# Kernel optimization log

Measured on AMD Instinct MI355X. Metric: run time of the kernel, lower is better.

The kernel has to match this reference:

```python
import jax
import jax.numpy as jnp
import numpy as np
from jax import lax

B, T, D = 32, 256, 512   # batch, seq len, controller_dim (== memory_dim)
S = 2048                 # memory_slots
EPS_LN = 1e-5            # nn.LayerNorm default eps
EPS_NRM = 1e-12          # F.normalize default eps


def setup_inputs() -> dict:
    key = jax.random.key(0)
    ks = jax.random.split(key, 12)
    sc = 1.0 / np.sqrt(D)  # roughly torch Linear init scale
    return {
        "controller_seq": jax.random.normal(ks[0], (B, T, D), dtype=jnp.float32),
        "memory": jax.random.normal(ks[1], (S, D), dtype=jnp.float32),
        "Wk": jax.random.normal(ks[2], (D, D), dtype=jnp.float32) * sc,
        "bk": jax.random.normal(ks[3], (D,), dtype=jnp.float32) * sc,
        "We": jax.random.normal(ks[4], (D, D), dtype=jnp.float32) * sc,
        "be": jax.random.normal(ks[5], (D,), dtype=jnp.float32) * sc,
        "Ww": jax.random.normal(ks[6], (D, D), dtype=jnp.float32) * sc,
        "bw": jax.random.normal(ks[7], (D,), dtype=jnp.float32) * sc,
        "Wg": jax.random.normal(ks[8], (D, D), dtype=jnp.float32) * sc,
        "bg": jax.random.normal(ks[9], (D,), dtype=jnp.float32) * sc,
        "gamma": jnp.ones((D,), dtype=jnp.float32),
        "beta": jnp.zeros((D,), dtype=jnp.float32),
    }


def _l2norm(x, axis=-1):
    # matches F.normalize: x / max(||x||, eps)
    n = jnp.sqrt(jnp.sum(x * x, axis=axis, keepdims=True))
    return x / jnp.maximum(n, EPS_NRM)


def _layernorm(x, gamma, beta):
    mu = jnp.mean(x, axis=-1, keepdims=True)
    var = jnp.mean((x - mu) ** 2, axis=-1, keepdims=True)
    return (x - mu) * lax.rsqrt(var + EPS_LN) * gamma + beta


def reference(controller_seq, memory, Wk, bk, We, be, Ww, bw, Wg, bg, gamma, beta):
    batch = controller_seq.shape[0]

    def step(mem, c):  # mem: [S, Dm], c: [B, Dc]
        # --- read (addressing by cosine similarity) ---
        k = c @ Wk.T + bk                       # [B, Dm]
        sim = _l2norm(k) @ _l2norm(mem).T       # [B, S]
        w = jax.nn.softmax(sim, axis=-1)        # [B, S]
        read_val = w @ mem                      # [B, Dm]
        # --- write (erase / add, averaged over batch) ---
        erase = jax.nn.sigmoid(c @ We.T + be)   # [B, Dm]
        add = c @ Ww.T + bw                     # [B, Dm]
        # mean_b (1 - w_bs * e_bd) = 1 - (w^T e)/B ; avoids [B,S,Dm] intermediate
        erase_m = 1.0 - jnp.einsum("bs,bd->sd", w, erase) / batch
        add_m = jnp.einsum("bs,bd->sd", w, add) / batch
        new_mem = _layernorm(mem * erase_m + add_m, gamma, beta)  # dropout in eval mode
        # --- gated output ---
        g = jax.nn.sigmoid(c @ Wg.T + bg)       # [B, Dm]
        out_t = g * c + (1.0 - g) * read_val
        return new_mem, out_t

    _, outs = lax.scan(step, memory, jnp.swapaxes(controller_seq, 0, 1))  # outs: [T, B, D]
    return jnp.swapaxes(outs, 0, 1)  # [B, T, D]
```

## Files before the change

kernel.cpp:

```cpp
#include <hip/hip_runtime.h>

#define DEV __device__ __forceinline__

namespace {
constexpr int Bc = 32;
constexpr int Tc = 256;
constexpr int Dc = 512;
constexpr int NBLK = 256;
constexpr int NW   = 128;
constexpr int ROWS = 16;

constexpr size_t OFF_KN   = 0;
constexpr size_t OFF_E    = OFF_KN + (size_t)Tc * Bc * Dc;
constexpr size_t OFF_A    = OFF_E  + (size_t)Tc * Bc * Dc;
constexpr size_t OFF_RP   = OFF_A  + (size_t)Tc * Bc * Dc;
constexpr size_t OFF_DENP = OFF_RP + (size_t)2 * NW * Bc * Dc;
constexpr size_t OFF_FLAGS= OFF_DENP + (size_t)2 * NW * Bc;
}

DEV float sigm(float x) { return 1.0f / (1.0f + __expf(-x)); }

DEV float ld1cg(const float* p) {
  unsigned u = __hip_atomic_load((const unsigned*)p, __ATOMIC_RELAXED,
                                 __HIP_MEMORY_SCOPE_AGENT);
  return __uint_as_float(u);
}
DEV void st1cg(float* p, float v) {
  __hip_atomic_store((unsigned*)p, __float_as_uint(v), __ATOMIC_RELAXED,
                     __HIP_MEMORY_SCOPE_AGENT);
}
DEV unsigned long long ld8cg(const unsigned long long* p) {
  return __hip_atomic_load(p, __ATOMIC_RELAXED, __HIP_MEMORY_SCOPE_AGENT);
}
DEV void st8cg(unsigned long long* p, unsigned long long v) {
  __hip_atomic_store(p, v, __ATOMIC_RELAXED, __HIP_MEMORY_SCOPE_AGENT);
}

DEV unsigned pack_bf2(float x, float y) {
  unsigned ux = __float_as_uint(x), uy = __float_as_uint(y);
  unsigned rx = (ux + 0x7FFFu + ((ux >> 16) & 1u)) >> 16;
  unsigned ry = (uy + 0x7FFFu + ((uy >> 16) & 1u)) >> 16;
  return rx | (ry << 16);
}
DEV float lo16f(unsigned u) { return __uint_as_float(u << 16); }
DEV float hi16f(unsigned u) { return __uint_as_float(u & 0xFFFF0000u); }

__global__ __launch_bounds__(256) void k_gemm(
    const float* __restrict__ A,
    const float* __restrict__ Wk, const float* __restrict__ bk,
    const float* __restrict__ We, const float* __restrict__ be,
    const float* __restrict__ Ww, const float* __restrict__ bw,
    const float* __restrict__ Wg, const float* __restrict__ bg,
    float* __restrict__ ws, float* __restrict__ gout)
{
  __shared__ float As[32][68];
  __shared__ float Bs[32][68];

  const int bid = blockIdx.x;
  const int mat = bid >> 10;
  const int rem = bid & 1023;
  const int rt = rem >> 3, jt = rem & 7;
  const int rbase = rt * 64, jbase = jt * 64;

  const float* Wm; const float* bm;
  if      (mat == 0) { Wm = Wk; bm = bk; }
  else if (mat == 1) { Wm = We; bm = be; }
  else if (mat == 2) { Wm = Ww; bm = bw; }
  else               { Wm = Wg; bm = bg; }

  const int tid = threadIdx.x;
  const int lr = tid >> 2;
  const int lk = (tid & 3) * 8;
  const int ty = tid >> 4, tx = tid & 15;

  float acc[4][4] = {};

  for (int k0 = 0; k0 < Dc; k0 += 32) {
    const float4 a0 = *(const float4*)&A [(size_t)(rbase + lr) * Dc + k0 + lk];
    const float4 a1 = *(const float4*)&A [(size_t)(rbase + lr) * Dc + k0 + lk + 4];
    const float4 b0 = *(const float4*)&Wm[(size_t)(jbase + lr) * Dc + k0 + lk];
    const float4 b1 = *(const float4*)&Wm[(size_t)(jbase + lr) * Dc + k0 + lk + 4];
    __syncthreads();
    As[lk + 0][lr] = a0.x; As[lk + 1][lr] = a0.y; As[lk + 2][lr] = a0.z; As[lk + 3][lr] = a0.w;
    As[lk + 4][lr] = a1.x; As[lk + 5][lr] = a1.y; As[lk + 6][lr] = a1.z; As[lk + 7][lr] = a1.w;
    Bs[lk + 0][lr] = b0.x; Bs[lk + 1][lr] = b0.y; Bs[lk + 2][lr] = b0.z; Bs[lk + 3][lr] = b0.w;
    Bs[lk + 4][lr] = b1.x; Bs[lk + 5][lr] = b1.y; Bs[lk + 6][lr] = b1.z; Bs[lk + 7][lr] = b1.w;
    __syncthreads();
    #pragma unroll
    for (int kk = 0; kk < 32; ++kk) {
      const float4 av = *(const float4*)&As[kk][ty * 4];
      const float4 bv = *(const float4*)&Bs[kk][tx * 4];
      const float ar[4] = {av.x, av.y, av.z, av.w};
      const float br[4] = {bv.x, bv.y, bv.z, bv.w};
      #pragma unroll
      for (int i = 0; i < 4; ++i)
        #pragma unroll
        for (int j = 0; j < 4; ++j)
          acc[i][j] = fmaf(ar[i], br[j], acc[i][j]);
    }
  }

  const float4 bias = *(const float4*)&bm[jbase + tx * 4];
  const float bi[4] = {bias.x, bias.y, bias.z, bias.w};
  #pragma unroll
  for (int i = 0; i < 4; ++i) {
    const int r = rbase + ty * 4 + i;
    float v[4];
    #pragma unroll
    for (int j = 0; j < 4; ++j) {
      v[j] = acc[i][j] + bi[j];
      if (mat & 1) v[j] = sigm(v[j]);
    }
    float4 o; o.x = v[0]; o.y = v[1]; o.z = v[2]; o.w = v[3];
    if (mat == 3) {
      *(float4*)&gout[(size_t)r * Dc + jbase + tx * 4] = o;
    } else {
      float* dst = ws + (mat == 0 ? OFF_KN : (mat == 1 ? OFF_E : OFF_A));
      const int t = r & 255, b = r >> 8;
      *(float4*)&dst[((size_t)t * Bc + b) * Dc + jbase + tx * 4] = o;
    }
  }
}

__global__ __launch_bounds__(256) void k_knorm(float* __restrict__ kn)
{
  const int row = blockIdx.x * 4 + (threadIdx.x >> 6);
  const int lane = threadIdx.x & 63;
  float* p = kn + (size_t)row * Dc;
  float4 v0 = *(const float4*)&p[lane * 4];
  float4 v1 = *(const float4*)&p[256 + lane * 4];
  float ss = v0.x*v0.x + v0.y*v0.y + v0.z*v0.z + v0.w*v0.w
           + v1.x*v1.x + v1.y*v1.y + v1.z*v1.z + v1.w*v1.w;
  #pragma unroll
  for (int off = 32; off >= 1; off >>= 1) ss += __shfl_xor(ss, off);
  const float inv = 1.0f / fmaxf(sqrtf(ss), 1e-12f);
  v0.x *= inv; v0.y *= inv; v0.z *= inv; v0.w *= inv;
  v1.x *= inv; v1.y *= inv; v1.z *= inv; v1.w *= inv;
  *(float4*)&p[lane * 4] = v0;
  *(float4*)&p[256 + lane * 4] = v1;
}

DEV void gbar(unsigned* flags, unsigned step, int bid, int tid)
{
  __syncthreads();
  if (tid == 0)
    __hip_atomic_store(&flags[bid * 16], step, __ATOMIC_RELAXED,
                       __HIP_MEMORY_SCOPE_AGENT);
  while (__hip_atomic_load(&flags[tid * 16], __ATOMIC_RELAXED,
                           __HIP_MEMORY_SCOPE_AGENT) < step)
    __builtin_amdgcn_s_sleep(1);
  __syncthreads();
}

DEV void sim_phase(const float* __restrict__ knp, float* __restrict__ denp_row,
                   const float (*y)[516], float* __restrict__ ew_own,
                   const float* invn_s, float* sred, int tid)
{
  const int r = tid >> 4, bp = tid & 15;
  const float* k0p = knp + (size_t)bp * Dc;
  const float* k1p = knp + (size_t)(bp + 16) * Dc;
  float acc0 = 0.f, acc1 = 0.f;
  #pragma unroll 4
  for (int dq = 0; dq < Dc / 4; ++dq) {
    const float4 y4 = *(const float4*)&y[r][dq * 4];
    const float4 ka = *(const float4*)&k0p[dq * 4];
    const float4 kb = *(const float4*)&k1p[dq * 4];
    acc0 = fmaf(y4.x, ka.x, acc0); acc0 = fmaf(y4.y, ka.y, acc0);
    acc0 = fmaf(y4.z, ka.z, acc0); acc0 = fmaf(y4.w, ka.w, acc0);
    acc1 = fmaf(y4.x, kb.x, acc1); acc1 = fmaf(y4.y, kb.y, acc1);
    acc1 = fmaf(y4.z, kb.z, acc1); acc1 = fmaf(y4.w, kb.w, acc1);
  }
  const float iv = invn_s[r];
  const float e0 = __expf(acc0 * iv);
  const float e1 = __expf(acc1 * iv);
  ew_own[r * 32 + bp]      = e0;
  ew_own[r * 32 + bp + 16] = e1;
  if (tid < 32) sred[tid] = 0.f;
  __syncthreads();
  atomicAdd(&sred[bp], e0);
  atomicAdd(&sred[bp + 16], e1);
  __syncthreads();
  if (tid < 32) st1cg(&denp_row[tid], sred[tid]);
}

__global__ __launch_bounds__(256, 1) void k_main(
    const float* __restrict__ cs, const float* __restrict__ mem_in,
    const float* __restrict__ gamma, const float* __restrict__ beta,
    float* __restrict__ ws, float* __restrict__ out)
{
  __shared__ float    mrows[16][516];
  __shared__ unsigned sbuf[32][256];
  __shared__ float    ew_own[16 * 32];
  __shared__ float    wbuf[16][32];
  __shared__ float    lds_red[256];
  __shared__ float    redR[16][128];
  __shared__ float    sred[32];
  __shared__ float    mu_s[16], rs_s[16], invn_s[16], dinv_s[32];

  float* kn   = ws + OFF_KN;
  float* eptb = ws + OFF_E;
  float* aptb = ws + OFF_A;
  unsigned long long* rp64_all = (unsigned long long*)(ws + OFF_RP);
  float* denp = ws + OFF_DENP;
  unsigned* flags = (unsigned*)(ws + OFF_FLAGS);

  const int bid = blockIdx.x, tid = threadIdx.x;
  const float inv32 = 1.0f / 32.0f;
  const size_t RPPAR = (size_t)NW * Bc * (Dc / 4);

  float2 ev[32], av[32];

  if (bid < NW) {
    const int s0 = bid * ROWS;
    const int c0 = tid * 2;
    #pragma unroll
    for (int r = 0; r < ROWS; ++r)
      *(float2*)&mrows[r][c0] = *(const float2*)&mem_in[(size_t)(s0 + r) * Dc + c0];
    #pragma unroll
    for (int b = 0; b < 32; ++b) {
      ev[b] = *(const float2*)&eptb[(size_t)b * Dc + c0];
      av[b] = *(const float2*)&aptb[(size_t)b * Dc + c0];
    }
    __syncthreads();
    {
      const int row = tid >> 4, li = tid & 15;
      float ss = 0.f;
      #pragma unroll
      for (int i = 0; i < 8; ++i) {
        const float4 v = *(const float4*)&mrows[row][(li + i * 16) * 4];
        ss += v.x*v.x + v.y*v.y + v.z*v.z + v.w*v.w;
      }
      ss += __shfl_xor(ss, 8); ss += __shfl_xor(ss, 4);
      ss += __shfl_xor(ss, 2); ss += __shfl_xor(ss, 1);
      if (li == 0) invn_s[row] = 1.0f / fmaxf(sqrtf(ss), 1e-12f);
    }
    __syncthreads();
    sim_phase(kn, denp + (size_t)bid * Bc, mrows, ew_own, invn_s, sred, tid);
  }
  gbar(flags, 1u, bid, tid);

  for (int t = 0; t <= Tc; ++t) {
    if (bid < NW) {
      if (t < Tc) {
        const int c0 = tid * 2;
        {
          const float* dp = denp + (size_t)(t & 1) * NW * Bc;
          const int b = tid & 31, ch = tid >> 5;
          float s = 0.f;
          #pragma unroll
          for (int g = 0; g < 16; ++g)
            s += ld1cg(&dp[(size_t)(ch * 16 + g) * Bc + b]);
          lds_red[tid] = s;
          __syncthreads();
          if (tid < 32) {
            float tot = 0.f;
            #pragma unroll
            for (int c2 = 0; c2 < 8; ++c2) tot += lds_red[c2 * 32 + tid];
            dinv_s[tid] = 1.0f / tot;
          }
          __syncthreads();
        }
        for (int idx = tid; idx < ROWS * 32; idx += 256)
          wbuf[idx >> 5][idx & 31] = ew_own[idx] * dinv_s[idx & 31];
        __syncthreads();

        float2 mr[ROWS];
        #pragma unroll
        for (int r = 0; r < ROWS; ++r) mr[r] = *(const float2*)&mrows[r][c0];
        #pragma unroll 4
        for (int b = 0; b < 32; ++b) {
          float2 a; a.x = 0.f; a.y = 0.f;
          #pragma unroll
          for (int r = 0; r < ROWS; ++r) {
            const float wv = wbuf[r][b];
            a.x = fmaf(wv, mr[r].x, a.x);
            a.y = fmaf(wv, mr[r].y, a.y);
          }
          sbuf[b][tid] = pack_bf2(a.x, a.y);
        }
        __syncthreads();
        {
          unsigned long long* rp64 = rp64_all + (size_t)(t & 1) * RPPAR
                                   + (size_t)bid * Bc * (Dc / 4);
          #pragma unroll
          for (int i = 0; i < 16; ++i) {
            const int idx = tid + i * 256;
            const int b = idx >> 7, dq = idx & 127;
            const unsigned long long v =
                (unsigned long long)sbuf[b][dq * 2]
              | ((unsigned long long)sbuf[b][dq * 2 + 1] << 32);
            st8cg(&rp64[(size_t)b * (Dc / 4) + dq], v);
          }
        }

        if (t < Tc - 1) {
          float2 er[ROWS] = {}, ad[ROWS] = {};
          #pragma unroll
          for (int b = 0; b < 32; ++b) {
            const float2 e2 = ev[b], a2 = av[b];
            #pragma unroll
            for (int r = 0; r < ROWS; ++r) {
              const float wv = wbuf[r][b];
              er[r].x = fmaf(wv, e2.x, er[r].x); er[r].y = fmaf(wv, e2.y, er[r].y);
              ad[r].x = fmaf(wv, a2.x, ad[r].x); ad[r].y = fmaf(wv, a2.y, ad[r].y);
            }
          }
          float2 xr[ROWS];
          #pragma unroll
          for (int r = 0; r < ROWS; ++r) {
            float2 x;
            x.x = mr[r].x * (1.0f - er[r].x * inv32) + ad[r].x * inv32;
            x.y = mr[r].y * (1.0f - er[r].y * inv32) + ad[r].y * inv32;
            xr[r] = x;
            *(float2*)&mrows[r][c0] = x;
          }
          if (t <= Tc - 3) {
            const float* ep1 = eptb + (size_t)(t + 1) * Bc * Dc;
            const float* ap1 = aptb + (size_t)(t + 1) * Bc * Dc;
            #pragma unroll
            for (int b = 0; b < 32; ++b) {
              ev[b] = *(const float2*)&ep1[(size_t)b * Dc + c0];
              av[b] = *(const float2*)&ap1[(size_t)b * Dc + c0];
            }
          }
          __syncthreads();
          {
            const int row = tid >> 4, li = tid & 15;
            float s1 = 0.f, s2 = 0.f;
            #pragma unroll
            for (int i = 0; i < 8; ++i) {
              const float4 v = *(const float4*)&mrows[row][(li + i * 16) * 4];
              s1 += v.x + v.y + v.z + v.w;
              s2 += v.x*v.x + v.y*v.y + v.z*v.z + v.w*v.w;
            }
            s1 += __shfl_xor(s1, 8); s2 += __shfl_xor(s2, 8);
            s1 += __shfl_xor(s1, 4); s2 += __shfl_xor(s2, 4);
            s1 += __shfl_xor(s1, 2); s2 += __shfl_xor(s2, 2);
            s1 += __shfl_xor(s1, 1); s2 += __shfl_xor(s2, 1);
            if (li == 0) {
              const float mu = s1 * (1.0f / 512.0f);
              const float var = s2 * (1.0f / 512.0f) - mu * mu;
              mu_s[row] = mu;
              rs_s[row] = rsqrtf(var + 1e-5f);
            }
          }
          __syncthreads();
          const float2 gm  = *(const float2*)&gamma[c0];
          const float2 bt2 = *(const float2*)&beta[c0];
          #pragma unroll
          for (int r = 0; r < ROWS; ++r) {
            const float mu = mu_s[r], rs = rs_s[r];
            float2 y;
            y.x = (xr[r].x - mu) * rs * gm.x + bt2.x;
            y.y = (xr[r].y - mu) * rs * gm.y + bt2.y;
            *(float2*)&mrows[r][c0] = y;
          }
          __syncthreads();
          {
            const int row = tid >> 4, li = tid & 15;
            float ss = 0.f;
            #pragma unroll
            for (int i = 0; i < 8; ++i) {
              const float4 v = *(const float4*)&mrows[row][(li + i * 16) * 4];
              ss += v.x*v.x + v.y*v.y + v.z*v.z + v.w*v.w;
            }
            ss += __shfl_xor(ss, 8); ss += __shfl_xor(ss, 4);
            ss += __shfl_xor(ss, 2); ss += __shfl_xor(ss, 1);
            if (li == 0) invn_s[row] = 1.0f / fmaxf(sqrtf(ss), 1e-12f);
          }
          __syncthreads();
          sim_phase(kn + (size_t)(t + 1) * Bc * Dc,
                    denp + (size_t)((t + 1) & 1) * NW * Bc + (size_t)bid * Bc,
                    mrows, ew_own, invn_s, sred, tid);
        }
      }
    } else {
      if (t >= 1) {
        const int t0 = t - 1;
        const int rb = bid - NW;
        const int b = rb >> 2;
        const int d0 = (rb & 3) * 128;
        const unsigned long long* rp64 = rp64_all + (size_t)(t0 & 1) * RPPAR;
        const int pg = tid >> 4;
        const int cq = tid & 15;
        const size_t cofs = (size_t)(d0 + cq * 8) / 4;
        float acc[8] = {};
        #pragma unroll
        for (int i = 0; i < 8; ++i) {
          const int p = pg * 8 + i;
          const size_t base = ((size_t)p * Bc + b) * (Dc / 4) + cofs;
          const unsigned long long v0 = ld8cg(&rp64[base]);
          const unsigned long long v1 = ld8cg(&rp64[base + 1]);
          const unsigned u0 = (unsigned)v0, u1 = (unsigned)(v0 >> 32);
          const unsigned u2 = (unsigned)v1, u3 = (unsigned)(v1 >> 32);
          acc[0] += lo16f(u0); acc[1] += hi16f(u0);
          acc[2] += lo16f(u1); acc[3] += hi16f(u1);
          acc[4] += lo16f(u2); acc[5] += hi16f(u2);
          acc[6] += lo16f(u3); acc[7] += hi16f(u3);
        }
        #pragma unroll
        for (int j = 0; j < 8; ++j) redR[pg][cq * 8 + j] = acc[j];
        __syncthreads();
        if (tid < 128) {
          float s = 0.f;
          #pragma unroll
          for (int p = 0; p < 16; ++p) s += redR[p][tid];
          const size_t oofs = ((size_t)b * Tc + t0) * Dc + d0 + tid;
          const float g  = out[oofs];
          const float cv = cs[oofs];
          out[oofs] = g * cv + (1.0f - g) * s;
        }
        __syncthreads();
      }
    }
    if (t < Tc) gbar(flags, (unsigned)(t + 2), bid, tid);
  }
}

extern "C" void kernel_launch(void* const* d_in, const int* in_sizes, int n_in,
                              void* d_out, int out_size, void* d_ws, size_t ws_size,
                              hipStream_t stream)
{
  const float* cs    = (const float*)d_in[0];
  const float* mem   = (const float*)d_in[1];
  const float* Wk    = (const float*)d_in[2];
  const float* bk    = (const float*)d_in[3];
  const float* We    = (const float*)d_in[4];
  const float* be    = (const float*)d_in[5];
  const float* Ww    = (const float*)d_in[6];
  const float* bw    = (const float*)d_in[7];
  const float* Wg    = (const float*)d_in[8];
  const float* bg    = (const float*)d_in[9];
  const float* gamma = (const float*)d_in[10];
  const float* beta  = (const float*)d_in[11];
  float* ws  = (float*)d_ws;
  float* out = (float*)d_out;

  hipMemsetAsync(ws + OFF_FLAGS, 0, 256 * 16 * sizeof(unsigned), stream);

  hipLaunchKernelGGL(k_gemm, dim3(4096), dim3(256), 0, stream,
                     cs, Wk, bk, We, be, Ww, bw, Wg, bg, ws, out);
  hipLaunchKernelGGL(k_knorm, dim3(2048), dim3(256), 0, stream, ws + OFF_KN);
  hipLaunchKernelGGL(k_main, dim3(NBLK), dim3(256), 0, stream,
                     cs, mem, gamma, beta, ws, out);
}
```

Before: 12.23 ms.

## Double threads per block in persistent kernel and store read partials as fp32

Raises the persistent k_main blocks from 256 to 512 threads, so each thread owns a single memory column instead of a pair. The per-step work is rewritten as one fused loop over rows that computes the read partials and the erase/add sums together. The bf16 packing of read partials through an LDS staging buffer is dropped in favour of direct fp32 stores, and the sim-phase LDS atomics are replaced by a plain column reduction. This aims for more latency hiding per CU and less packing and sync overhead, at the cost of twice the partial-buffer traffic and possibly higher register pressure with launch bounds (512,2).

```diff
diff --git a/kernel.cpp b/kernel.cpp
--- a/kernel.cpp
+++ b/kernel.cpp
@@ -9,6 +9,7 @@
 constexpr int NBLK = 256;
 constexpr int NW   = 128;
 constexpr int ROWS = 16;
+constexpr int NT   = 512;
 
 constexpr size_t OFF_KN   = 0;
 constexpr size_t OFF_E    = OFF_KN + (size_t)Tc * Bc * Dc;
@@ -29,21 +30,6 @@
   __hip_atomic_store((unsigned*)p, __float_as_uint(v), __ATOMIC_RELAXED,
                      __HIP_MEMORY_SCOPE_AGENT);
 }
-DEV unsigned long long ld8cg(const unsigned long long* p) {
-  return __hip_atomic_load(p, __ATOMIC_RELAXED, __HIP_MEMORY_SCOPE_AGENT);
-}
-DEV void st8cg(unsigned long long* p, unsigned long long v) {
-  __hip_atomic_store(p, v, __ATOMIC_RELAXED, __HIP_MEMORY_SCOPE_AGENT);
-}
-
-DEV unsigned pack_bf2(float x, float y) {
-  unsigned ux = __float_as_uint(x), uy = __float_as_uint(y);
-  unsigned rx = (ux + 0x7FFFu + ((ux >> 16) & 1u)) >> 16;
-  unsigned ry = (uy + 0x7FFFu + ((uy >> 16) & 1u)) >> 16;
-  return rx | (ry << 16);
-}
-DEV float lo16f(unsigned u) { return __uint_as_float(u << 16); }
-DEV float hi16f(unsigned u) { return __uint_as_float(u & 0xFFFF0000u); }
 
 __global__ __launch_bounds__(256) void k_gemm(
     const float* __restrict__ A,
@@ -146,197 +132,180 @@
   if (tid == 0)
     __hip_atomic_store(&flags[bid * 16], step, __ATOMIC_RELAXED,
                        __HIP_MEMORY_SCOPE_AGENT);
-  while (__hip_atomic_load(&flags[tid * 16], __ATOMIC_RELAXED,
-                           __HIP_MEMORY_SCOPE_AGENT) < step)
-    __builtin_amdgcn_s_sleep(1);
+  if (tid < 256) {
+    while (__hip_atomic_load(&flags[tid * 16], __ATOMIC_RELAXED,
+                             __HIP_MEMORY_SCOPE_AGENT) < step)
+      __builtin_amdgcn_s_sleep(1);
+  }
   __syncthreads();
 }
 
 DEV void sim_phase(const float* __restrict__ knp, float* __restrict__ denp_row,
                    const float (*y)[516], float* __restrict__ ew_own,
-                   const float* invn_s, float* sred, int tid)
-{
-  const int r = tid >> 4, bp = tid & 15;
-  const float* k0p = knp + (size_t)bp * Dc;
-  const float* k1p = knp + (size_t)(bp + 16) * Dc;
-  float acc0 = 0.f, acc1 = 0.f;
+                   const float* invn_s, int tid)
+{
+  const int r = tid >> 5, bp = tid & 31;
+  const float* kp = knp + (size_t)bp * Dc;
+  float acc = 0.f;
   #pragma unroll 4
   for (int dq = 0; dq < Dc / 4; ++dq) {
     const float4 y4 = *(const float4*)&y[r][dq * 4];
-    const float4 ka = *(const float4*)&k0p[dq * 4];
-    const float4 kb = *(const float4*)&k1p[dq * 4];
-    acc0 = fmaf(y4.x, ka.x, acc0); acc0 = fmaf(y4.y, ka.y, acc0);
-    acc0 = fmaf(y4.z, ka.z, acc0); acc0 = fmaf(y4.w, ka.w, acc0);
-    acc1 = fmaf(y4.x, kb.x, acc1); acc1 = fmaf(y4.y, kb.y, acc1);
-    acc1 = fmaf(y4.z, kb.z, acc1); acc1 = fmaf(y4.w, kb.w, acc1);
-  }
-  const float iv = invn_s[r];
-  const float e0 = __expf(acc0 * iv);
-  const float e1 = __expf(acc1 * iv);
-  ew_own[r * 32 + bp]      = e0;
-  ew_own[r * 32 + bp + 16] = e1;
-  if (tid < 32) sred[tid] = 0.f;
+    const float4 k4 = *(const float4*)&kp[dq * 4];
+    acc = fmaf(y4.x, k4.x, acc); acc = fmaf(y4.y, k4.y, acc);
+    acc = fmaf(y4.z, k4.z, acc); acc = fmaf(y4.w, k4.w, acc);
+  }
+  ew_own[tid] = __expf(acc * invn_s[r]);
   __syncthreads();
-  atomicAdd(&sred[bp], e0);
-  atomicAdd(&sred[bp + 16], e1);
-  __syncthreads();
-  if (tid < 32) st1cg(&denp_row[tid], sred[tid]);
-}
-
-__global__ __launch_bounds__(256, 1) void k_main(
+  if (tid < 32) {
+    float s = 0.f;
+    #pragma unroll
+    for (int r2 = 0; r2 < 16; ++r2) s += ew_own[r2 * 32 + tid];
+    st1cg(&denp_row[tid], s);
+  }
+}
+
+__global__ __launch_bounds__(512, 2) void k_main(
     const float* __restrict__ cs, const float* __restrict__ mem_in,
     const float* __restrict__ gamma, const float* __restrict__ beta,
     float* __restrict__ ws, float* __restrict__ out)
 {
-  __shared__ float    mrows[16][516];
-  __shared__ unsigned sbuf[32][256];
-  __shared__ float    ew_own[16 * 32];
-  __shared__ float    wbuf[16][32];
-  __shared__ float    lds_red[256];
-  __shared__ float    redR[16][128];
-  __shared__ float    sred[32];
-  __shared__ float    mu_s[16], rs_s[16], invn_s[16], dinv_s[32];
+  __shared__ float mrows[16][516];
+  __shared__ float ew_own[512];
+  __shared__ float wbuf[16][32];
+  __shared__ float lds_red[512];
+  __shared__ float mu_s[16], rs_s[16], invn_s[16], dinv_s[32];
 
   float* kn   = ws + OFF_KN;
   float* eptb = ws + OFF_E;
   float* aptb = ws + OFF_A;
-  unsigned long long* rp64_all = (unsigned long long*)(ws + OFF_RP);
+  float* rp   = ws + OFF_RP;
   float* denp = ws + OFF_DENP;
   unsigned* flags = (unsigned*)(ws + OFF_FLAGS);
 
   const int bid = blockIdx.x, tid = threadIdx.x;
   const float inv32 = 1.0f / 32.0f;
-  const size_t RPPAR = (size_t)NW * Bc * (Dc / 4);
-
-  float2 ev[32], av[32];
+  const size_t RPPAR = (size_t)NW * Bc * Dc;
+
+  float ev[32], av[32];
+  const float gmv = gamma[tid & 511];
+  const float btv = beta[tid & 511];
 
   if (bid < NW) {
     const int s0 = bid * ROWS;
-    const int c0 = tid * 2;
     #pragma unroll
     for (int r = 0; r < ROWS; ++r)
-      *(float2*)&mrows[r][c0] = *(const float2*)&mem_in[(size_t)(s0 + r) * Dc + c0];
+      mrows[r][tid] = mem_in[(size_t)(s0 + r) * Dc + tid];
     #pragma unroll
     for (int b = 0; b < 32; ++b) {
-      ev[b] = *(const float2*)&eptb[(size_t)b * Dc + c0];
-      av[b] = *(const float2*)&aptb[(size_t)b * Dc + c0];
+      ev[b] = eptb[(size_t)b * Dc + tid];
+      av[b] = aptb[(size_t)b * Dc + tid];
     }
     __syncthreads();
     {
-      const int row = tid >> 4, li = tid & 15;
+      const int row = tid >> 5, li = tid & 31;
       float ss = 0.f;
       #pragma unroll
-      for (int i = 0; i < 8; ++i) {
-        const float4 v = *(const float4*)&mrows[row][(li + i * 16) * 4];
+      for (int i = 0; i < 4; ++i) {
+        const float4 v = *(const float4*)&mrows[row][(li + i * 32) * 4];
         ss += v.x*v.x + v.y*v.y + v.z*v.z + v.w*v.w;
       }
-      ss += __shfl_xor(ss, 8); ss += __shfl_xor(ss, 4);
-      ss += __shfl_xor(ss, 2); ss += __shfl_xor(ss, 1);
+      ss += __shfl_xor(ss, 16); ss += __shfl_xor(ss, 8);
+      ss += __shfl_xor(ss, 4);  ss += __shfl_xor(ss, 2);
+      ss += __shfl_xor(ss, 1);
       if (li == 0) invn_s[row] = 1.0f / fmaxf(sqrtf(ss), 1e-12f);
     }
     __syncthreads();
-    sim_phase(kn, denp + (size_t)bid * Bc, mrows, ew_own, invn_s, sred, tid);
+    sim_phase(kn, denp + (size_t)bid * Bc, mrows, ew_own, invn_s, tid);
   }
   gbar(flags, 1u, bid, tid);
 
   for (int t = 0; t <= Tc; ++t) {
     if (bid < NW) {
       if (t < Tc) {
-        const int c0 = tid * 2;
         {
           const float* dp = denp + (size_t)(t & 1) * NW * Bc;
-          const int b = tid & 31, ch = tid >> 5;
+          const int ch = tid >> 5, b = tid & 31;
           float s = 0.f;
           #pragma unroll
-          for (int g = 0; g < 16; ++g)
-            s += ld1cg(&dp[(size_t)(ch * 16 + g) * Bc + b]);
+          for (int g = 0; g < 8; ++g)
+            s += ld1cg(&dp[(size_t)(ch * 8 + g) * Bc + b]);
           lds_red[tid] = s;
           __syncthreads();
           if (tid < 32) {
             float tot = 0.f;
             #pragma unroll
-            for (int c2 = 0; c2 < 8; ++c2) tot += lds_red[c2 * 32 + tid];
+            for (int c2 = 0; c2 < 16; ++c2) tot += lds_red[c2 * 32 + tid];
             dinv_s[tid] = 1.0f / tot;
           }
           __syncthreads();
         }
-        for (int idx = tid; idx < ROWS * 32; idx += 256)
-          wbuf[idx >> 5][idx & 31] = ew_own[idx] * dinv_s[idx & 31];
+        wbuf[tid >> 5][tid & 31] = ew_own[tid] * dinv_s[tid & 31];
         __syncthreads();
 
-        float2 mr[ROWS];
+        float mr[16];
         #pragma unroll
-        for (int r = 0; r < ROWS; ++r) mr[r] = *(const float2*)&mrows[r][c0];
-        #pragma unroll 4
-        for (int b = 0; b < 32; ++b) {
-          float2 a; a.x = 0.f; a.y = 0.f;
+        for (int r = 0; r < ROWS; ++r) mr[r] = mrows[r][tid];
+        float rpv[32] = {};
+        float er[16] = {}, ad[16] = {};
+        #pragma unroll
+        for (int r = 0; r < ROWS; ++r) {
+          const float mrr = mr[r];
+          #pragma unroll
+          for (int b4 = 0; b4 < 8; ++b4) {
+            const float4 w4 = *(const float4*)&wbuf[r][b4 * 4];
+            rpv[b4*4+0] = fmaf(w4.x, mrr, rpv[b4*4+0]);
+            rpv[b4*4+1] = fmaf(w4.y, mrr, rpv[b4*4+1]);
+            rpv[b4*4+2] = fmaf(w4.z, mrr, rpv[b4*4+2]);
+            rpv[b4*4+3] = fmaf(w4.w, mrr, rpv[b4*4+3]);
+            er[r] = fmaf(w4.x, ev[b4*4+0], er[r]);
+            er[r] = fmaf(w4.y, ev[b4*4+1], er[r]);
+            er[r] = fmaf(w4.z, ev[b4*4+2], er[r]);
+            er[r] = fmaf(w4.w, ev[b4*4+3], er[r]);
+            ad[r] = fmaf(w4.x, av[b4*4+0], ad[r]);
+            ad[r] = fmaf(w4.y, av[b4*4+1], ad[r]);
+            ad[r] = fmaf(w4.z, av[b4*4+2], ad[r]);
+            ad[r] = fmaf(w4.w, av[b4*4+3], ad[r]);
+          }
+        }
+        {
+          float* rpd = rp + (size_t)(t & 1) * RPPAR
+                     + (size_t)bid * Bc * Dc + tid;
+          #pragma unroll
+          for (int b = 0; b < 32; ++b) st1cg(&rpd[(size_t)b * Dc], rpv[b]);
+        }
+
+        if (t < Tc - 1) {
+          float xr[16];
           #pragma unroll
           for (int r = 0; r < ROWS; ++r) {
-            const float wv = wbuf[r][b];
-            a.x = fmaf(wv, mr[r].x, a.x);
-            a.y = fmaf(wv, mr[r].y, a.y);
-          }
-          sbuf[b][tid] = pack_bf2(a.x, a.y);
-        }
-        __syncthreads();
-        {
-          unsigned long long* rp64 = rp64_all + (size_t)(t & 1) * RPPAR
-                                   + (size_t)bid * Bc * (Dc / 4);
-          #pragma unroll
-          for (int i = 0; i < 16; ++i) {
-            const int idx = tid + i * 256;
-            const int b = idx >> 7, dq = idx & 127;
-            const unsigned long long v =
-                (unsigned long long)sbuf[b][dq * 2]
-              | ((unsigned long long)sbuf[b][dq * 2 + 1] << 32);
-            st8cg(&rp64[(size_t)b * (Dc / 4) + dq], v);
-          }
-        }
-
-        if (t < Tc - 1) {
-          float2 er[ROWS] = {}, ad[ROWS] = {};
-          #pragma unroll
-          for (int b = 0; b < 32; ++b) {
-            const float2 e2 = ev[b], a2 = av[b];
-            #pragma unroll
-            for (int r = 0; r < ROWS; ++r) {
-              const float wv = wbuf[r][b];
-              er[r].x = fmaf(wv, e2.x, er[r].x); er[r].y = fmaf(wv, e2.y, er[r].y);
-              ad[r].x = fmaf(wv, a2.x, ad[r].x); ad[r].y = fmaf(wv, a2.y, ad[r].y);
-            }
-          }
-          float2 xr[ROWS];
-          #pragma unroll
-          for (int r = 0; r < ROWS; ++r) {
-            float2 x;
-            x.x = mr[r].x * (1.0f - er[r].x * inv32) + ad[r].x * inv32;
-            x.y = mr[r].y * (1.0f - er[r].y * inv32) + ad[r].y * inv32;
+            const float x = mr[r] * (1.0f - er[r] * inv32) + ad[r] * inv32;
             xr[r] = x;
-            *(float2*)&mrows[r][c0] = x;
+            mrows[r][tid] = x;
           }
           if (t <= Tc - 3) {
             const float* ep1 = eptb + (size_t)(t + 1) * Bc * Dc;
             const float* ap1 = aptb + (size_t)(t + 1) * Bc * Dc;
             #pragma unroll
             for (int b = 0; b < 32; ++b) {
-              ev[b] = *(const float2*)&ep1[(size_t)b * Dc + c0];
-              av[b] = *(const float2*)&ap1[(size_t)b * Dc + c0];
+              ev[b] = ep1[(size_t)b * Dc + tid];
+              av[b] = ap1[(size_t)b * Dc + tid];
             }
           }
           __syncthreads();
           {
-            const int row = tid >> 4, li = tid & 15;
+            const int row = tid >> 5, li = tid & 31;
             float s1 = 0.f, s2 = 0.f;
             #pragma unroll
-            for (int i = 0; i < 8; ++i) {
-              const float4 v = *(const float4*)&mrows[row][(li + i * 16) * 4];
+            for (int i = 0; i < 4; ++i) {
+              const float4 v = *(const float4*)&mrows[row][(li + i * 32) * 4];
               s1 += v.x + v.y + v.z + v.w;
               s2 += v.x*v.x + v.y*v.y + v.z*v.z + v.w*v.w;
             }
-            s1 += __shfl_xor(s1, 8); s2 += __shfl_xor(s2, 8);
-            s1 += __shfl_xor(s1, 4); s2 += __shfl_xor(s2, 4);
-            s1 += __shfl_xor(s1, 2); s2 += __shfl_xor(s2, 2);
-            s1 += __shfl_xor(s1, 1); s2 += __shfl_xor(s2, 1);
+            s1 += __shfl_xor(s1, 16); s2 += __shfl_xor(s2, 16);
+            s1 += __shfl_xor(s1, 8);  s2 += __shfl_xor(s2, 8);
+            s1 += __shfl_xor(s1, 4);  s2 += __shfl_xor(s2, 4);
+            s1 += __shfl_xor(s1, 2);  s2 += __shfl_xor(s2, 2);
+            s1 += __shfl_xor(s1, 1);  s2 += __shfl_xor(s2, 1);
             if (li == 0) {
               const float mu = s1 * (1.0f / 512.0f);
               const float var = s2 * (1.0f / 512.0f) - mu * mu;
@@ -345,33 +314,29 @@
             }
           }
           __syncthreads();
-          const float2 gm  = *(const float2*)&gamma[c0];
-          const float2 bt2 = *(const float2*)&beta[c0];
           #pragma unroll
           for (int r = 0; r < ROWS; ++r) {
-            const float mu = mu_s[r], rs = rs_s[r];
-            float2 y;
-            y.x = (xr[r].x - mu) * rs * gm.x + bt2.x;
-            y.y = (xr[r].y - mu) * rs * gm.y + bt2.y;
-            *(float2*)&mrows[r][c0] = y;
+            const float y = (xr[r] - mu_s[r]) * rs_s[r] * gmv + btv;
+            mrows[r][tid] = y;
           }
           __syncthreads();
           {
-            const int row = tid >> 4, li = tid & 15;
+            const int row = tid >> 5, li = tid & 31;
             float ss = 0.f;
             #pragma unroll
-            for (int i = 0; i < 8; ++i) {
-              const float4 v = *(const float4*)&mrows[row][(li + i * 16) * 4];
+            for (int i = 0; i < 4; ++i) {
+              const float4 v = *(const float4*)&mrows[row][(li + i * 32) * 4];
               ss += v.x*v.x + v.y*v.y + v.z*v.z + v.w*v.w;
             }
-            ss += __shfl_xor(ss, 8); ss += __shfl_xor(ss, 4);
-            ss += __shfl_xor(ss, 2); ss += __shfl_xor(ss, 1);
+            ss += __shfl_xor(ss, 16); ss += __shfl_xor(ss, 8);
+            ss += __shfl_xor(ss, 4);  ss += __shfl_xor(ss, 2);
+            ss += __shfl_xor(ss, 1);
             if (li == 0) invn_s[row] = 1.0f / fmaxf(sqrtf(ss), 1e-12f);
           }
           __syncthreads();
           sim_phase(kn + (size_t)(t + 1) * Bc * Dc,
                     denp + (size_t)((t + 1) & 1) * NW * Bc + (size_t)bid * Bc,
-                    mrows, ew_own, invn_s, sred, tid);
+                    mrows, ew_own, invn_s, tid);
         }
       }
     } else {
@@ -380,31 +345,20 @@
         const int rb = bid - NW;
         const int b = rb >> 2;
         const int d0 = (rb & 3) * 128;
-        const unsigned long long* rp64 = rp64_all + (size_t)(t0 & 1) * RPPAR;
-        const int pg = tid >> 4;
-        const int cq = tid & 15;
-        const size_t cofs = (size_t)(d0 + cq * 8) / 4;
-        float acc[8] = {};
-        #pragma unroll
-        for (int i = 0; i < 8; ++i) {
-          const int p = pg * 8 + i;
-          const size_t base = ((size_t)p * Bc + b) * (Dc / 4) + cofs;
-          const unsigned long long v0 = ld8cg(&rp64[base]);
-          const unsigned long long v1 = ld8cg(&rp64[base + 1]);
-          const unsigned u0 = (unsigned)v0, u1 = (unsigned)(v0 >> 32);
-          const unsigned u2 = (unsigned)v1, u3 = (unsigned)(v1 >> 32);
-          acc[0] += lo16f(u0); acc[1] += hi16f(u0);
-          acc[2] += lo16f(u1); acc[3] += hi16f(u1);
-          acc[4] += lo16f(u2); acc[5] += hi16f(u2);
-          acc[6] += lo16f(u3); acc[7] += hi16f(u3);
-        }
-        #pragma unroll
-        for (int j = 0; j < 8; ++j) redR[pg][cq * 8 + j] = acc[j];
+        const float* rpp = rp + (size_t)(t0 & 1) * RPPAR;
+        const int pg = tid >> 7;
+        const int c  = tid & 127;
+        float acc = 0.f;
+        #pragma unroll 4
+        for (int i = 0; i < 32; ++i) {
+          const int p = pg * 32 + i;
+          acc += ld1cg(&rpp[((size_t)p * Bc + b) * Dc + d0 + c]);
+        }
+        lds_red[pg * 128 + c] = acc;
         __syncthreads();
         if (tid < 128) {
-          float s = 0.f;
-          #pragma unroll
-          for (int p = 0; p < 16; ++p) s += redR[p][tid];
+          const float s = lds_red[tid] + lds_red[128 + tid]
+                        + lds_red[256 + tid] + lds_red[384 + tid];
           const size_t oofs = ((size_t)b * Tc + t0) * Dc + d0 + tid;
           const float g  = out[oofs];
           const float cv = cs[oofs];
@@ -441,6 +395,6 @@
   hipLaunchKernelGGL(k_gemm, dim3(4096), dim3(256), 0, stream,
                      cs, Wk, bk, We, be, Ww, bw, Wg, bg, ws, out);
   hipLaunchKernelGGL(k_knorm, dim3(2048), dim3(256), 0, stream, ws + OFF_KN);
-  hipLaunchKernelGGL(k_main, dim3(NBLK), dim3(256), 0, stream,
+  hipLaunchKernelGGL(k_main, dim3(NBLK), dim3(NT), 0, stream,
                      cs, mem, gamma, beta, ws, out);
 }
```

New measurement: 30.57 ms. 150% more time.
